# Performance work log

Measured on AMD Instinct MI355X. Metric: run time of the kernel, lower is better.

The kernel has to match this reference:

```python
import jax, jax.numpy as jnp
import numpy as np

E, T, K, N = 8, 8192, 2048, 4096  # experts, total tokens, hidden, ffn-out


def setup_inputs() -> dict:
    key = jax.random.key(0)
    k1, k2, k3, k4 = jax.random.split(key, 4)
    a = jax.random.normal(k1, (T, K), dtype=jnp.float32)
    # weight_column_major=True layout: [num_experts, N, K]
    b = jax.random.normal(k2, (E, N, K), dtype=jnp.float32) * 0.02
    c = jnp.zeros((T, N), dtype=jnp.float32)  # preallocated output buffer
    # monotone segment offsets: 0 = p0 <= p1 <= ... <= pE = T
    cuts = jnp.sort(jax.random.randint(k3, (E - 1,), 0, T))
    seg_indptr = jnp.concatenate([
        jnp.zeros((1,), jnp.int64),
        cuts.astype(jnp.int64),
        jnp.full((1,), T, jnp.int64),
    ])
    weight_indices = jax.random.permutation(k4, E).astype(jnp.int64)
    return {
        "a": a,
        "b": b,
        "c": c,
        "batch_size": E,
        "weight_column_major": 1,
        "seg_indptr": seg_indptr,
        "weight_indices": weight_indices,
    }


def reference(a, b, c, batch_size, weight_column_major, seg_indptr, weight_indices):
    # Grouped GEMM: for each segment s, c[p_s:p_{s+1}] = a[p_s:p_{s+1}] @ b[widx[s]].T
    group_sizes = jnp.diff(seg_indptr).astype(jnp.int32)  # [E]
    # gather per-segment weights and convert column-major [E,N,K] -> [E,K,N]
    rhs = jnp.swapaxes(b[weight_indices], 1, 2)
    return jax.lax.ragged_dot(a, rhs, group_sizes)  # [T, N]
```

## Files before the change

### kernel.cpp

```cpp
#include <hip/hip_runtime.h>
#include <stdint.h>
#include <stddef.h>


typedef __attribute__((ext_vector_type(8))) short short8;
typedef __attribute__((ext_vector_type(4))) float floatx4;

constexpr int E_c = 8;
constexpr int T_c = 8192;
constexpr int K_c = 2048;
constexpr int N_c = 4096;
constexpr int BM = 128;
constexpr int BN = 128;
constexpr int BK = 32;
constexpr int KSTEPS = K_c / BK;
constexpr int XTILES = T_c / BM + E_c;
constexpr int YTILES = N_c / BN;
constexpr int LSTR = 5;

__device__ __forceinline__ uint32_t pack2(float lo, float hi) {
  union { float f; uint32_t u; } a, b;
  a.f = lo; b.f = hi;
  return __builtin_amdgcn_perm(b.u, a.u, 0x07060302u);
}

__device__ __forceinline__ void cvt16(const float4* p, int4* c0, int4* c1) {
  c0->x = pack2(p[0].x, p[0].y); c0->y = pack2(p[0].z, p[0].w);
  c0->z = pack2(p[1].x, p[1].y); c0->w = pack2(p[1].z, p[1].w);
  c1->x = pack2(p[2].x, p[2].y); c1->y = pack2(p[2].z, p[2].w);
  c1->z = pack2(p[3].x, p[3].y); c1->w = pack2(p[3].z, p[3].w);
}

__global__ __launch_bounds__(256) void grouped_gemm_kernel(
    const float* __restrict__ A, const float* __restrict__ B,
    const int* __restrict__ segp, const int* __restrict__ widx,
    float* __restrict__ C) {
  __shared__ int4 As[BM * LSTR];
  __shared__ int4 Bs[BN * LSTR];

  const int t = threadIdx.x;

  const int bid = blockIdx.x;
  const int xcd = bid & 7;
  const int i = bid >> 3;
  const int yl = i / XTILES;
  const int x = i - yl * XTILES;
  const int y = xcd * 4 + yl;

  int s = -1, r0i = 0, rendi = 0, acc_t = 0;
#pragma unroll
  for (int e = 0; e < E_c; ++e) {
    int pe = segp[e], pe1 = segp[e + 1];
    int nt = (pe1 - pe + BM - 1) >> 7;
    if (s < 0 && (x - acc_t) < nt) {
      s = e;
      r0i = pe + ((x - acc_t) << 7);
      rendi = pe1;
    }
    acc_t += nt;
  }
  if (s < 0) return;
  const int expert = widx[s];
  const int n0 = y * BN;

  const int r = t >> 1;
  const int h = t & 1;
  int arow = r0i + r;
  if (arow > T_c - 1) arow = T_c - 1;
  const float* Abase = A + (size_t)arow * K_c + h * 16;
  const float* Bbase = B + ((size_t)expert * N_c + n0 + r) * K_c + h * 16;
  const int wI = r * LSTR + 2 * h;

  const int lane = t & 63;
  const int wave = t >> 6;
  const int m16 = lane & 15;
  const int quad = lane >> 4;
  const int wm = (wave & 1) << 6;
  const int wn = (wave >> 1) << 6;
  int ia[4], ib[4];
#pragma unroll
  for (int q = 0; q < 4; ++q) {
    ia[q] = (wm + q * 16 + m16) * LSTR + quad;
    ib[q] = (wn + q * 16 + m16) * LSTR + quad;
  }

  floatx4 acc[4][4];
#pragma unroll
  for (int p = 0; p < 4; ++p)
#pragma unroll
    for (int q = 0; q < 4; ++q) acc[p][q] = (floatx4){0.f, 0.f, 0.f, 0.f};

  float4 pa[4], pb[4];
#pragma unroll
  for (int j = 0; j < 4; ++j) {
    pa[j] = ((const float4*)Abase)[j];
    pb[j] = ((const float4*)Bbase)[j];
  }

#pragma unroll 1
  for (int kt = 0; kt < KSTEPS; ++kt) {
    __syncthreads();
    int4 a0, a1, b0, b1;
    cvt16(pa, &a0, &a1);
    cvt16(pb, &b0, &b1);
    As[wI] = a0; As[wI + 1] = a1;
    Bs[wI] = b0; Bs[wI + 1] = b1;
    __syncthreads();

    const int knext = (kt + 1 < KSTEPS) ? kt + 1 : KSTEPS - 1;
    const float* an = Abase + knext * BK;
    const float* bn = Bbase + knext * BK;
#pragma unroll
    for (int j = 0; j < 4; ++j) {
      pa[j] = ((const float4*)an)[j];
      pb[j] = ((const float4*)bn)[j];
    }

    short8 aF[4], bF[4];
#pragma unroll
    for (int q = 0; q < 4; ++q) {
      aF[q] = *(const short8*)&As[ia[q]];
      bF[q] = *(const short8*)&Bs[ib[q]];
    }
#pragma unroll
    for (int p = 0; p < 4; ++p)
#pragma unroll
      for (int q = 0; q < 4; ++q)
        acc[p][q] = __builtin_amdgcn_mfma_f32_16x16x32_bf16(aF[p], bF[q],
                                                            acc[p][q], 0, 0, 0);
  }

#pragma unroll
  for (int p = 0; p < 4; ++p) {
    int growb = r0i + wm + p * 16 + quad * 4;
#pragma unroll
    for (int q = 0; q < 4; ++q) {
      int gcol = n0 + wn + q * 16 + m16;
#pragma unroll
      for (int rr = 0; rr < 4; ++rr) {
        int grow = growb + rr;
        if (grow < rendi) C[(size_t)grow * N_c + gcol] = acc[p][q][rr];
      }
    }
  }
}

extern "C" void kernel_launch(void* const* d_in, const int* in_sizes, int n_in,
                              void* d_out, int out_size, void* d_ws, size_t ws_size,
                              hipStream_t stream) {
  const float* A = (const float*)d_in[0];
  const float* B = (const float*)d_in[1];
  const int* segp = (const int*)d_in[5];
  const int* widx = (const int*)d_in[6];
  float* C = (float*)d_out;

  grouped_gemm_kernel<<<dim3(XTILES * YTILES), 256, 0, stream>>>(A, B, segp,
                                                                 widx, C);
}
```

Before: 793.5 us.

## Pre-convert A and B to bf16 in workspace and load tiles via global_load_lds

Adds separate conversion kernels that turn A and all expert weights into bf16 in the workspace. The GEMM then streams bf16 tiles directly into LDS with global_load_lds, dropping the per-step register conversion and halving operand bytes read inside the GEMM. In exchange it pays an extra full pass that reads fp32 and writes bf16 for both A and B. The new LDS layout is unpadded, which may cause bank conflicts, and the old fp32 kernel is kept as a fallback when the workspace is too small.

Result: faster. 723.1 us (-8.9%).

```diff
diff --git a/kernel.cpp b/kernel.cpp
--- a/kernel.cpp
+++ b/kernel.cpp
@@ -16,7 +16,6 @@
 constexpr int KSTEPS = K_c / BK;
 constexpr int XTILES = T_c / BM + E_c;
 constexpr int YTILES = N_c / BN;
-constexpr int LSTR = 5;
 
 __device__ __forceinline__ uint32_t pack2(float lo, float hi) {
   union { float f; uint32_t u; } a, b;
@@ -24,19 +23,34 @@
   return __builtin_amdgcn_perm(b.u, a.u, 0x07060302u);
 }
 
-__device__ __forceinline__ void cvt16(const float4* p, int4* c0, int4* c1) {
-  c0->x = pack2(p[0].x, p[0].y); c0->y = pack2(p[0].z, p[0].w);
-  c0->z = pack2(p[1].x, p[1].y); c0->w = pack2(p[1].z, p[1].w);
-  c1->x = pack2(p[2].x, p[2].y); c1->y = pack2(p[2].z, p[2].w);
-  c1->z = pack2(p[3].x, p[3].y); c1->w = pack2(p[3].z, p[3].w);
-}
-
-__global__ __launch_bounds__(256) void grouped_gemm_kernel(
-    const float* __restrict__ A, const float* __restrict__ B,
+__global__ __launch_bounds__(256) void cvt_bf16_kernel(
+    const float* __restrict__ src, ushort* __restrict__ dst, int n8) {
+  int i = blockIdx.x * 256 + threadIdx.x;
+  const int stride = gridDim.x * 256;
+  for (; i < n8; i += stride) {
+    const float4* p = (const float4*)src + (size_t)i * 2;
+    float4 v0 = p[0], v1 = p[1];
+    int4 o;
+    o.x = pack2(v0.x, v0.y);
+    o.y = pack2(v0.z, v0.w);
+    o.z = pack2(v1.x, v1.y);
+    o.w = pack2(v1.z, v1.w);
+    ((int4*)dst)[i] = o;
+  }
+}
+
+__device__ __forceinline__ void gload16(const ushort* g, ushort* l) {
+  __builtin_amdgcn_global_load_lds(
+      (const __attribute__((address_space(1))) unsigned int*)g,
+      (__attribute__((address_space(3))) unsigned int*)l, 16, 0, 0);
+}
+
+__global__ __launch_bounds__(256) void grouped_gemm_bf16_kernel(
+    const ushort* __restrict__ A, const ushort* __restrict__ B,
     const int* __restrict__ segp, const int* __restrict__ widx,
     float* __restrict__ C) {
-  __shared__ int4 As[BM * LSTR];
-  __shared__ int4 Bs[BN * LSTR];
+  __shared__ ushort As[BM * BK];
+  __shared__ ushort Bs[BN * BK];
 
   const int t = threadIdx.x;
 
@@ -63,6 +77,122 @@
   const int expert = widx[s];
   const int n0 = y * BN;
 
+  const int wave = t >> 6;
+  const int lane = t & 63;
+  const int rl = lane >> 2;
+  const int kq = lane & 3;
+
+  int ar0 = r0i + wave * 16 + rl;
+  int ar1 = ar0 + 64;
+  if (ar0 > T_c - 1) ar0 = T_c - 1;
+  if (ar1 > T_c - 1) ar1 = T_c - 1;
+  const ushort* Ag0 = A + (size_t)ar0 * K_c + kq * 8;
+  const ushort* Ag1 = A + (size_t)ar1 * K_c + kq * 8;
+  const ushort* Bg0 =
+      B + ((size_t)expert * N_c + n0 + wave * 16 + rl) * K_c + kq * 8;
+  const ushort* Bg1 = Bg0 + (size_t)64 * K_c;
+
+  ushort* Al0 = As + wave * 512;
+  ushort* Al1 = As + 2048 + wave * 512;
+  ushort* Bl0 = Bs + wave * 512;
+  ushort* Bl1 = Bs + 2048 + wave * 512;
+
+  const int m16 = lane & 15;
+  const int quad = lane >> 4;
+  const int wm = (wave & 1) << 6;
+  const int wn = (wave >> 1) << 6;
+  int ia[4], ib[4];
+#pragma unroll
+  for (int q = 0; q < 4; ++q) {
+    ia[q] = (wm + q * 16 + m16) * BK + quad * 8;
+    ib[q] = (wn + q * 16 + m16) * BK + quad * 8;
+  }
+
+  floatx4 acc[4][4];
+#pragma unroll
+  for (int p = 0; p < 4; ++p)
+#pragma unroll
+    for (int q = 0; q < 4; ++q) acc[p][q] = (floatx4){0.f, 0.f, 0.f, 0.f};
+
+#pragma unroll 1
+  for (int kt = 0; kt < KSTEPS; ++kt) {
+    __syncthreads();
+    gload16(Ag0, Al0);
+    gload16(Ag1, Al1);
+    gload16(Bg0, Bl0);
+    gload16(Bg1, Bl1);
+    Ag0 += BK; Ag1 += BK; Bg0 += BK; Bg1 += BK;
+    __syncthreads();
+
+    short8 aF[4], bF[4];
+#pragma unroll
+    for (int q = 0; q < 4; ++q) {
+      aF[q] = *(const short8*)&As[ia[q]];
+      bF[q] = *(const short8*)&Bs[ib[q]];
+    }
+#pragma unroll
+    for (int p = 0; p < 4; ++p)
+#pragma unroll
+      for (int q = 0; q < 4; ++q)
+        acc[p][q] = __builtin_amdgcn_mfma_f32_16x16x32_bf16(aF[p], bF[q],
+                                                            acc[p][q], 0, 0, 0);
+  }
+
+#pragma unroll
+  for (int p = 0; p < 4; ++p) {
+    int growb = r0i + wm + p * 16 + quad * 4;
+#pragma unroll
+    for (int q = 0; q < 4; ++q) {
+      int gcol = n0 + wn + q * 16 + m16;
+#pragma unroll
+      for (int rr = 0; rr < 4; ++rr) {
+        int grow = growb + rr;
+        if (grow < rendi) C[(size_t)grow * N_c + gcol] = acc[p][q][rr];
+      }
+    }
+  }
+}
+
+constexpr int LSTR = 5;
+
+__device__ __forceinline__ void cvt16(const float4* p, int4* c0, int4* c1) {
+  c0->x = pack2(p[0].x, p[0].y); c0->y = pack2(p[0].z, p[0].w);
+  c0->z = pack2(p[1].x, p[1].y); c0->w = pack2(p[1].z, p[1].w);
+  c1->x = pack2(p[2].x, p[2].y); c1->y = pack2(p[2].z, p[2].w);
+  c1->z = pack2(p[3].x, p[3].y); c1->w = pack2(p[3].z, p[3].w);
+}
+
+__global__ __launch_bounds__(256) void grouped_gemm_fallback(
+    const float* __restrict__ A, const float* __restrict__ B,
+    const int* __restrict__ segp, const int* __restrict__ widx,
+    float* __restrict__ C) {
+  __shared__ int4 As[BM * LSTR];
+  __shared__ int4 Bs[BN * LSTR];
+
+  const int t = threadIdx.x;
+  const int bid = blockIdx.x;
+  const int xcd = bid & 7;
+  const int i = bid >> 3;
+  const int yl = i / XTILES;
+  const int x = i - yl * XTILES;
+  const int y = xcd * 4 + yl;
+
+  int s = -1, r0i = 0, rendi = 0, acc_t = 0;
+#pragma unroll
+  for (int e = 0; e < E_c; ++e) {
+    int pe = segp[e], pe1 = segp[e + 1];
+    int nt = (pe1 - pe + BM - 1) >> 7;
+    if (s < 0 && (x - acc_t) < nt) {
+      s = e;
+      r0i = pe + ((x - acc_t) << 7);
+      rendi = pe1;
+    }
+    acc_t += nt;
+  }
+  if (s < 0) return;
+  const int expert = widx[s];
+  const int n0 = y * BN;
+
   const int r = t >> 1;
   const int h = t & 1;
   int arow = r0i + r;
@@ -98,7 +228,7 @@
   }
 
 #pragma unroll 1
-  for (int kt = 0; kt < KSTEPS; ++kt) {
+  for (int kt = 0; kt < KSTEPS * BK / 32; ++kt) {
     __syncthreads();
     int4 a0, a1, b0, b1;
     cvt16(pa, &a0, &a1);
@@ -107,9 +237,9 @@
     Bs[wI] = b0; Bs[wI + 1] = b1;
     __syncthreads();
 
-    const int knext = (kt + 1 < KSTEPS) ? kt + 1 : KSTEPS - 1;
-    const float* an = Abase + knext * BK;
-    const float* bn = Bbase + knext * BK;
+    const int knext = (kt + 1 < 64) ? kt + 1 : 63;
+    const float* an = Abase + knext * 32;
+    const float* bn = Bbase + knext * 32;
 #pragma unroll
     for (int j = 0; j < 4; ++j) {
       pa[j] = ((const float4*)an)[j];
@@ -154,6 +284,18 @@
   const int* widx = (const int*)d_in[6];
   float* C = (float*)d_out;
 
-  grouped_gemm_kernel<<<dim3(XTILES * YTILES), 256, 0, stream>>>(A, B, segp,
-                                                                 widx, C);
-}
+  const size_t abytes = (size_t)T_c * K_c * 2;
+  const size_t bbytes = (size_t)E_c * N_c * K_c * 2;
+
+  if (ws_size >= abytes + bbytes) {
+    ushort* Abf = (ushort*)d_ws;
+    ushort* Bbf = Abf + (size_t)T_c * K_c;
+    cvt_bf16_kernel<<<2048, 256, 0, stream>>>(A, Abf, T_c * K_c / 8);
+    cvt_bf16_kernel<<<2048, 256, 0, stream>>>(B, Bbf, E_c * N_c * K_c / 8);
+    grouped_gemm_bf16_kernel<<<dim3(XTILES * YTILES), 256, 0, stream>>>(
+        Abf, Bbf, segp, widx, C);
+  } else {
+    grouped_gemm_fallback<<<dim3(XTILES * YTILES), 256, 0, stream>>>(
+        A, B, segp, widx, C);
+  }
+}
```
